# Optimization experiments

Measured on AMD Instinct MI355X. Metric: run time of the kernel, lower is better.

Reference implementation:

```python
import jax, jax.numpy as jnp
import numpy as np

B = 32            # graphs in batch
NPG = 2048        # nodes per graph (equal-size graphs -> static topk sizes)
N = B * NPG
DEG = 8
E = N * DEG
IN = 64
H1 = 2 * IN       # 128
H2 = 2 * H1       # 256
K1 = NPG // 2     # SAGPooling ratio=0.5
K2 = K1 // 2
EPS = 1e-5


def _lin(k, fi, fo):
    s = 1.0 / np.sqrt(fi)
    return jax.random.uniform(k, (fi, fo), jnp.float32, -s, s)


def setup_inputs() -> dict:
    key = jax.random.key(0)
    ks = jax.random.split(key, 24)
    x = jax.random.normal(ks[0], (N, IN), jnp.float32)
    # edges strictly within each graph
    eg = jnp.repeat(jnp.arange(B, dtype=jnp.int32), NPG * DEG)
    src = eg * NPG + jax.random.randint(ks[1], (E,), 0, NPG, jnp.int32)
    tgt = eg * NPG + jax.random.randint(ks[2], (E,), 0, NPG, jnp.int32)
    edge_index = jnp.stack([src, tgt])
    batch = jnp.repeat(jnp.arange(B, dtype=jnp.int32), NPG)
    return {
        "x": x, "edge_index": edge_index, "batch": batch,
        # SAGEConv1: lin_l (neighbors, with bias) + lin_r (root, no bias)
        "W1l": _lin(ks[3], IN, H1), "b1l": jnp.zeros((H1,), jnp.float32),
        "W1r": _lin(ks[4], IN, H1),
        "bn1_g": jnp.ones((H1,), jnp.float32), "bn1_b": jnp.zeros((H1,), jnp.float32),
        # SAGPooling1 scorer = GraphConv(H1, 1): lin_rel (sum-agg, bias) + lin_root
        "p1_Wrel": _lin(ks[5], H1, 1), "p1_brel": jnp.zeros((1,), jnp.float32),
        "p1_Wroot": _lin(ks[6], H1, 1),
        "W2l": _lin(ks[7], H1, H2), "b2l": jnp.zeros((H2,), jnp.float32),
        "W2r": _lin(ks[8], H1, H2),
        "bn2_g": jnp.ones((H2,), jnp.float32), "bn2_b": jnp.zeros((H2,), jnp.float32),
        "p2_Wrel": _lin(ks[9], H2, 1), "p2_brel": jnp.zeros((1,), jnp.float32),
        "p2_Wroot": _lin(ks[10], H2, 1),
        "Wlin": _lin(ks[11], H2, 2), "blin": jnp.zeros((2,), jnp.float32),
    }


def sage_conv(x, src, tgt, emask, Wl, bl, Wr, n):
    # PyG SAGEConv: mean-aggregate x_j over valid incoming edges, then lin_l(agg)+lin_r(x)
    msg = x[src] * emask[:, None]
    s = jax.ops.segment_sum(msg, tgt, num_segments=n)
    cnt = jax.ops.segment_sum(emask, tgt, num_segments=n)
    mean = s / jnp.maximum(cnt, 1.0)[:, None]
    return mean @ Wl + bl + x @ Wr


def graph_conv_score(x, src, tgt, emask, Wrel, brel, Wroot, n):
    # PyG GraphConv (sum aggregation), out_channels=1
    s = jax.ops.segment_sum(x[src] * emask[:, None], tgt, num_segments=n)
    return (s @ Wrel + brel + x @ Wroot)[:, 0]


def batch_norm(x, g, b):
    m = x.mean(0)
    v = jnp.mean((x - m) ** 2, 0)  # biased var, as BatchNorm1d training
    return (x - m) * jax.lax.rsqrt(v + EPS) * g + b


def sag_pool(x, src, tgt, emask, score, npg, k):
    # per-graph top-k by score; x_kept scaled by tanh(score); edges re-filtered via mask
    vals, idx = jax.lax.top_k(score.reshape(B, npg), k)          # [B,k]
    perm = (jnp.arange(B, dtype=jnp.int32)[:, None] * npg + idx.astype(jnp.int32)).reshape(-1)
    xnew = x[perm] * jnp.tanh(vals.reshape(-1))[:, None]
    mapping = jnp.full((x.shape[0],), -1, jnp.int32).at[perm].set(
        jnp.arange(B * k, dtype=jnp.int32))
    ns, nt = mapping[src], mapping[tgt]
    valid = emask * ((ns >= 0) & (nt >= 0)).astype(emask.dtype)
    return xnew, jnp.maximum(ns, 0), jnp.maximum(nt, 0), valid


def reference(x, edge_index, batch, W1l, b1l, W1r, bn1_g, bn1_b,
              p1_Wrel, p1_brel, p1_Wroot, W2l, b2l, W2r, bn2_g, bn2_b,
              p2_Wrel, p2_brel, p2_Wroot, Wlin, blin):
    src, tgt = edge_index[0], edge_index[1]
    emask = jnp.ones((src.shape[0],), x.dtype)

    h = sage_conv(x, src, tgt, emask, W1l, b1l, W1r, N)
    h = jax.nn.relu(batch_norm(h, bn1_g, bn1_b))
    s1 = graph_conv_score(h, src, tgt, emask, p1_Wrel, p1_brel, p1_Wroot, N)
    h, src, tgt, emask = sag_pool(h, src, tgt, emask, s1, NPG, K1)

    n1 = B * K1
    h = sage_conv(h, src, tgt, emask, W2l, b2l, W2r, n1)
    h = jax.nn.relu(batch_norm(h, bn2_g, bn2_b))
    s2 = graph_conv_score(h, src, tgt, emask, p2_Wrel, p2_brel, p2_Wroot, n1)
    h, src, tgt, emask = sag_pool(h, src, tgt, emask, s2, K1, K2)

    batch2 = jnp.repeat(jnp.arange(B, dtype=jnp.int32), K2)
    pooled = jax.ops.segment_sum(h, batch2, num_segments=B) / jnp.asarray(K2, h.dtype)
    out = jax.nn.relu(pooled) @ Wlin + blin
    return jax.nn.softmax(out, axis=1)
```

## Files before the change

### kernel.cpp

```cpp
#include <hip/hip_runtime.h>
#include <math.h>

#define Bg   32
#define NPGc 2048
#define Nn   (Bg*NPGc)
#define DEGc 8
#define Ee   (Nn*DEGc)
#define INc  64
#define H1c  128
#define H2c  256
#define K1c  1024
#define K2c  512
#define N1c  (Bg*K1c)
#define N2c  (Bg*K2c)
#define SLAB 64

typedef __attribute__((ext_vector_type(8))) short short8;
typedef __attribute__((ext_vector_type(4))) float f32x4;

__device__ __forceinline__ ushort f2bf(float f) {
    uint u = __float_as_uint(f);
    uint r = (u + 0x7fffu + ((u >> 16) & 1u)) >> 16;
    return (ushort)r;
}
__device__ __forceinline__ float bf2f(ushort v) { return __uint_as_float((uint)v << 16); }
__device__ __forceinline__ float bfhi(uint v) { return __uint_as_float(v & 0xffff0000u); }
__device__ __forceinline__ float bflo(uint v) { return __uint_as_float(v << 16); }
__device__ __forceinline__ uint fkey(float f) {
    uint u = __float_as_uint(f);
    return u ^ ((uint)((int)u >> 31) | 0x80000000u);
}
__device__ __forceinline__ void unpk8(uint4 v, float* f) {
    f[0] = bflo(v.x); f[1] = bfhi(v.x);
    f[2] = bflo(v.y); f[3] = bfhi(v.y);
    f[4] = bflo(v.z); f[5] = bfhi(v.z);
    f[6] = bflo(v.w); f[7] = bfhi(v.w);
}
__device__ __forceinline__ uint4 pack8(const float* a, float inv) {
    uint4 o;
    o.x = (uint)f2bf(a[0] * inv) | ((uint)f2bf(a[1] * inv) << 16);
    o.y = (uint)f2bf(a[2] * inv) | ((uint)f2bf(a[3] * inv) << 16);
    o.z = (uint)f2bf(a[4] * inv) | ((uint)f2bf(a[5] * inv) << 16);
    o.w = (uint)f2bf(a[6] * inv) | ((uint)f2bf(a[7] * inv) << 16);
    return o;
}
__device__ __forceinline__ void accf8(float* a, const float* p) {
    float4 u0 = *(const float4*)p;
    float4 u1 = *(const float4*)(p + 4);
    a[0] += u0.x; a[1] += u0.y; a[2] += u0.z; a[3] += u0.w;
    a[4] += u1.x; a[5] += u1.y; a[6] += u1.z; a[7] += u1.w;
}

__global__ void init_kernel(int4* __restrict__ wc1, int4* __restrict__ dstats) {
    int id = blockIdx.x * blockDim.x + threadIdx.x;
    int4 z = {0, 0, 0, 0};
    if (id < 16384) { wc1[id] = z; return; }
    id -= 16384;
    if (id < 384)   { dstats[id] = z; }
}
#define INIT_TOTAL (16384 + 384)

__global__ void prep2_kernel(const int* __restrict__ src, const int* __restrict__ tgt,
                             const float* __restrict__ W1l, const float* __restrict__ W1r,
                             const float* __restrict__ W2l, const float* __restrict__ W2r,
                             ushort* __restrict__ T1l, ushort* __restrict__ T1r,
                             ushort* __restrict__ T2l, ushort* __restrict__ T2r,
                             int* __restrict__ wc1, int* __restrict__ col1) {
    int id = blockIdx.x * blockDim.x + threadIdx.x;
    if (id < Ee) {
        int t = tgt[id];
        int p = atomicAdd(&wc1[t], 1);
        col1[t * SLAB + p] = src[id];
        return;
    }
    id -= Ee;
    if (id < 8192) {
        int c = id / 64, k = id % 64;
        T1l[id] = f2bf(W1l[k * 128 + c]);
        T1r[id] = f2bf(W1r[k * 128 + c]);
        return;
    }
    id -= 8192;
    if (id < 32768) {
        int c = id / 128, k = id % 128;
        T2l[id] = f2bf(W2l[k * 256 + c]);
        T2r[id] = f2bf(W2r[k * 256 + c]);
    }
}
#define PREP2_TOTAL (Ee + 8192 + 32768)

__global__ __launch_bounds__(512) void gemm1f_kernel(
        const float* __restrict__ x, const int* __restrict__ deg,
        const int* __restrict__ col, const ushort* __restrict__ Wtl,
        const ushort* __restrict__ Wtr, const float* __restrict__ bias,
        ushort* __restrict__ out, double* __restrict__ dsum,
        double* __restrict__ dsq) {
    __shared__ ushort As[2][2][128][36];
    __shared__ ushort Bs[2][2][128][36];
    __shared__ float bsumS[2][128], bsqS[2][128];
    int b = blockIdx.x;
    int bs = ((b & 7) << 6) + (b >> 3);
    int m0 = bs << 7;
    int lane = threadIdx.x & 63;
    int wid = threadIdx.x >> 6;
    int wr = (wid & 1) << 6, wc = (wid >> 1) << 5;
    int l16 = lane & 15, quad = lane >> 4;

    int ar = threadIdx.x >> 2, ack = (threadIdx.x & 3) * 8;
    int anode = m0 + ar;
    int abg = anode * SLAB, adg = deg[anode];
    int4 c0h = *(const int4*)&col[abg];
    int4 c1h = *(const int4*)&col[abg + 4];
    int anb[8] = {c0h.x, c0h.y, c0h.z, c0h.w, c1h.x, c1h.y, c1h.z, c1h.w};

    {
        int r = threadIdx.x >> 2, ck = (threadIdx.x & 3) * 8;
#pragma unroll
        for (int kt = 0; kt < 2; kt++) {
            *(uint4*)&Bs[0][kt][r][ck] = *(const uint4*)&Wtl[(size_t)r * INc + kt * 32 + ck];
            *(uint4*)&Bs[1][kt][r][ck] = *(const uint4*)&Wtr[(size_t)r * INc + kt * 32 + ck];
        }
    }
    {
#pragma unroll
        for (int kt = 0; kt < 2; kt++) {
            const float* xp = &x[(size_t)anode * INc + kt * 32 + ack];
            float vals[8];
            float4 v0 = *(const float4*)xp, v1 = *(const float4*)(xp + 4);
            vals[0] = v0.x; vals[1] = v0.y; vals[2] = v0.z; vals[3] = v0.w;
            vals[4] = v1.x; vals[5] = v1.y; vals[6] = v1.z; vals[7] = v1.w;
            *(uint4*)&As[1][kt][ar][ack] = pack8(vals, 1.f);
        }
    }
    {
        float aacc[2][8];
#pragma unroll
        for (int kt = 0; kt < 2; kt++)
#pragma unroll
            for (int q = 0; q < 8; q++) aacc[kt][q] = 0.f;
#pragma unroll
        for (int j = 0; j < 8; j++)
            if (j < adg) {
                const float* xp = &x[(size_t)anb[j] * INc + ack];
#pragma unroll
                for (int kt = 0; kt < 2; kt++) accf8(aacc[kt], xp + kt * 32);
            }
        for (int i = abg + 8; i < abg + adg; i++) {
            const float* xp = &x[(size_t)col[i] * INc + ack];
#pragma unroll
            for (int kt = 0; kt < 2; kt++) accf8(aacc[kt], xp + kt * 32);
        }
        int cdg = adg < 1 ? 1 : adg;
        float inv = 1.f / (float)cdg;
#pragma unroll
        for (int kt = 0; kt < 2; kt++)
            *(uint4*)&As[0][kt][ar][ack] = pack8(aacc[kt], inv);
    }
    __syncthreads();

    f32x4 acc[4][2];
#pragma unroll
    for (int a = 0; a < 4; a++)
#pragma unroll
        for (int c = 0; c < 2; c++) acc[a][c] = (f32x4){0.f, 0.f, 0.f, 0.f};

#pragma unroll
    for (int kt = 0; kt < 2; kt++) {
        short8 a[2][4], bfr[2][2];
#pragma unroll
        for (int s = 0; s < 2; s++)
#pragma unroll
            for (int mt = 0; mt < 4; mt++)
                a[s][mt] = *(const short8*)&As[s][kt][wr + mt * 16 + l16][quad * 8];
#pragma unroll
        for (int s = 0; s < 2; s++)
#pragma unroll
            for (int nt = 0; nt < 2; nt++)
                bfr[s][nt] = *(const short8*)&Bs[s][kt][wc + nt * 16 + l16][quad * 8];
#pragma unroll
        for (int mt = 0; mt < 4; mt++)
#pragma unroll
            for (int nt = 0; nt < 2; nt++) {
                acc[mt][nt] = __builtin_amdgcn_mfma_f32_16x16x32_bf16(
                    a[0][mt], bfr[0][nt], acc[mt][nt], 0, 0, 0);
                acc[mt][nt] = __builtin_amdgcn_mfma_f32_16x16x32_bf16(
                    a[1][mt], bfr[1][nt], acc[mt][nt], 0, 0, 0);
            }
    }
    float s[2] = {0.f, 0.f}, sq[2] = {0.f, 0.f};
#pragma unroll
    for (int nt = 0; nt < 2; nt++) {
        int colx = wc + nt * 16 + l16;
        float bv = bias[colx];
#pragma unroll
        for (int mt = 0; mt < 4; mt++)
#pragma unroll
            for (int rr = 0; rr < 4; rr++) {
                int row = m0 + wr + mt * 16 + quad * 4 + rr;
                float ov = acc[mt][nt][rr] + bv;
                out[(size_t)row * H1c + colx] = f2bf(ov);
                s[nt] += ov; sq[nt] += ov * ov;
            }
    }
#pragma unroll
    for (int nt = 0; nt < 2; nt++) {
        float ss = s[nt], qq = sq[nt];
        ss += __shfl_down(ss, 16); qq += __shfl_down(qq, 16);
        ss += __shfl_down(ss, 32); qq += __shfl_down(qq, 32);
        if (quad == 0) {
            bsumS[wid & 1][wc + nt * 16 + l16] = ss;
            bsqS[wid & 1][wc + nt * 16 + l16] = qq;
        }
    }
    __syncthreads();
    if (threadIdx.x < 128) {
        int c = threadIdx.x;
        atomicAdd(&dsum[c], (double)(bsumS[0][c] + bsumS[1][c]));
        atomicAdd(&dsq[c], (double)(bsqS[0][c] + bsqS[1][c]));
    }
}

template<int C>
__global__ __launch_bounds__(256) void score_kernel(const ushort* __restrict__ h,
                                                    const double* __restrict__ dsum,
                                                    const double* __restrict__ dsq,
                                                    const float* __restrict__ g,
                                                    const float* __restrict__ b,
                                                    const float* __restrict__ wrel,
                                                    const float* __restrict__ wroot,
                                                    float* __restrict__ r,
                                                    float* __restrict__ root, int n) {
    __shared__ float sc[C], sh[C], wrl[C], wrt[C];
    if ((int)threadIdx.x < C) {
        int c = threadIdx.x;
        double m = dsum[c] / (double)n;
        double var = dsq[c] / (double)n - m * m;
        float s = g[c] * (float)(1.0 / sqrt(var + 1e-5));
        sc[c] = s; sh[c] = b[c] - (float)m * s;
        wrl[c] = wrel[c]; wrt[c] = wroot[c];
    }
    __syncthreads();
    int gid = blockIdx.x * 256 + threadIdx.x;
    int node = gid >> 3, ln = gid & 7;
    float rr = 0.f, rt = 0.f;
#pragma unroll
    for (int p = 0; p < C / 64; p++) {
        int cb = p * 64 + ln * 8;
        uint4 v = *(const uint4*)&h[(size_t)node * C + cb];
        float vv[8];
        unpk8(v, vv);
#pragma unroll
        for (int q = 0; q < 8; q++) {
            int cc = cb + q;
            float val = fmaxf(vv[q] * sc[cc] + sh[cc], 0.f);
            rr += val * wrl[cc];
            rt += val * wrt[cc];
        }
    }
#pragma unroll
    for (int off = 4; off; off >>= 1) {
        rr += __shfl_down(rr, off);
        rt += __shfl_down(rt, off);
    }
    if (ln == 0) { r[node] = rr; root[node] = rt; }
}

__global__ void __launch_bounds__(1024) sel1_kernel(const float* __restrict__ r,
                                                    const float* __restrict__ root,
                                                    const int* __restrict__ deg,
                                                    const int* __restrict__ col,
                                                    const float* __restrict__ brel,
                                                    int* __restrict__ perm,
                                                    float* __restrict__ tval,
                                                    int* __restrict__ map) {
    __shared__ float rL[2048];
    __shared__ float svals[2048];
    __shared__ uint hist[257];
    __shared__ uint wsum[16];
    __shared__ uint s_b, s_rem;
    int g = blockIdx.x;
    int tid = threadIdx.x;
    int lane = tid & 63, wid = tid >> 6;
    int base = g * NPGc;
    rL[tid] = r[base + tid];
    rL[tid + 1024] = r[base + tid + 1024];
    if (tid < 257) hist[tid] = 0;
    __syncthreads();
    float bv = brel[0];
#pragma unroll
    for (int j = 0; j < 2; j++) {
        int i = tid + (j << 10);
        int node = base + i;
        float acc = bv + root[node];
        int e0 = node * SLAB, dg = deg[node];
        int4 c0 = *(const int4*)&col[e0];
        int4 c1 = *(const int4*)&col[e0 + 4];
        int nb[8] = {c0.x, c0.y, c0.z, c0.w, c1.x, c1.y, c1.z, c1.w};
#pragma unroll
        for (int q = 0; q < 8; q++)
            if (q < dg) acc += rL[nb[q] - base];
        for (int e = e0 + 8; e < e0 + dg; e++) acc += rL[col[e] - base];
        svals[i] = acc;
    }
    __syncthreads();

    uint prefix = 0, himask = 0, rem = (uint)K1c;
    for (int shift = 24; shift >= 0; shift -= 8) {
#pragma unroll
        for (int j = 0; j < 2; j++) {
            uint kk = fkey(svals[tid + (j << 10)]);
            if ((kk & himask) == prefix) atomicAdd(&hist[(kk >> shift) & 255], 1);
        }
        __syncthreads();
        if (tid < 64) {
            int L = tid;
            uint h0 = hist[4 * L], h1v = hist[4 * L + 1], h2v = hist[4 * L + 2],
                 h3 = hist[4 * L + 3];
            uint s3 = h3, s2 = h2v + s3, s1 = h1v + s2, s0 = h0 + s1;
            uint v = s0;
            for (int off = 1; off < 64; off <<= 1) {
                uint u = __shfl_down(v, off);
                if (L + off < 64) v += u;
            }
            uint above = v - s0;
            hist[4 * L] = s0 + above;
            hist[4 * L + 1] = s1 + above;
            hist[4 * L + 2] = s2 + above;
            hist[4 * L + 3] = s3 + above;
        }
        __syncthreads();
        if (tid < 256) {
            uint sb = hist[tid], sb1 = hist[tid + 1];
            if (sb >= rem && sb1 < rem) { s_b = (uint)tid; s_rem = rem - sb1; }
        }
        __syncthreads();
        prefix |= (s_b << shift);
        rem = s_rem;
        himask |= (0xFFu << shift);
        if (tid < 256) hist[tid] = 0;
        __syncthreads();
    }
    uint thr = prefix;
    uint tieM = rem;
    uint gcnt = 0, ecnt = 0, gflags = 0, eflags = 0;
#pragma unroll
    for (int j = 0; j < 2; j++) {
        uint kk = fkey(svals[tid + (j << 10)]);
        if (kk > thr) { gflags |= 1u << j; gcnt++; }
        else if (kk == thr) { eflags |= 1u << j; ecnt++; }
    }
    uint key = (gcnt << 16) | ecnt;
    uint v = key;
    for (int off = 1; off < 64; off <<= 1) {
        uint u = __shfl_up(v, off);
        if (lane >= off) v += u;
    }
    if (lane == 63) wsum[wid] = v;
    __syncthreads();
    if (tid < 16) {
        uint w0 = wsum[tid], w = w0;
        for (int off = 1; off < 16; off <<= 1) {
            uint u = __shfl_up(w, off);
            if ((int)tid >= off) w += u;
        }
        wsum[tid] = w - w0;
    }
    __syncthreads();
    uint excl = (v - key) + wsum[wid];
    uint gbase = excl >> 16, ebase = excl & 0xFFFFu;
#pragma unroll
    for (int j = 0; j < 2; j++) {
        bool gt = (gflags >> j) & 1u;
        bool eq = (eflags >> j) & 1u;
        int i = tid + (j << 10);
        int o = -1;
        if (gt || (eq && ebase < tieM)) {
            uint pos = gbase + min(ebase, tieM);
            o = g * K1c + (int)pos;
            perm[o] = base + i;
            tval[o] = tanhf(svals[i]);
        }
        map[base + i] = o;
        gbase += gt ? 1u : 0u;
        ebase += eq ? 1u : 0u;
    }
}

__global__ void __launch_bounds__(256) nofill2_kernel(
        const int* __restrict__ perm1, const int* __restrict__ map1,
        const int* __restrict__ deg1, const int* __restrict__ col1,
        int* __restrict__ wc2, int* __restrict__ col2) {
    int n = blockIdx.x * 256 + threadIdx.x;
    int o = perm1[n];
    int e0 = o * SLAB, dg = deg1[o];
    int4 c0 = *(const int4*)&col1[e0];
    int4 c1 = *(const int4*)&col1[e0 + 4];
    int nb[8] = {c0.x, c0.y, c0.z, c0.w, c1.x, c1.y, c1.z, c1.w};
    int cnt = 0;
    int ob = n * SLAB;
#pragma unroll
    for (int j = 0; j < 8; j++) {
        if (j < dg) {
            int m = map1[nb[j]];
            if (m >= 0) col2[ob + cnt++] = m;
        }
    }
    for (int e = e0 + 8; e < e0 + dg; e++) {
        int m = map1[col1[e]];
        if (m >= 0) col2[ob + cnt++] = m;
    }
    wc2[n] = cnt;
}

__global__ __launch_bounds__(512) void gemm2f_kernel(
        const ushort* __restrict__ h1, const int* __restrict__ perm1,
        const float* __restrict__ tv1, const double* __restrict__ dsum1,
        const double* __restrict__ dsq1, const float* __restrict__ bn1g,
        const float* __restrict__ bn1b, const int* __restrict__ deg,
        const int* __restrict__ col, const ushort* __restrict__ Wtl,
        const ushort* __restrict__ Wtr, const float* __restrict__ bias,
        ushort* __restrict__ out, double* __restrict__ dsum,
        double* __restrict__ dsq) {
    __shared__ ushort As[2][4][128][36];
    __shared__ ushort Bs[2][2][256][36];
    __shared__ float bsumS[2][256], bsqS[2][256];
    __shared__ float sc1[128], sh1[128];
    int b = blockIdx.x;
    int bs = ((b & 7) << 5) + (b >> 3);
    int m0 = bs << 7;
    int lane = threadIdx.x & 63;
    int wid = threadIdx.x >> 6;
    int wr = (wid & 1) << 6, wc = (wid >> 1) << 6;
    int l16 = lane & 15, quad = lane >> 4;

    if (threadIdx.x < 128) {
        int c = threadIdx.x;
        double m = dsum1[c] / (double)Nn;
        double var = dsq1[c] / (double)Nn - m * m;
        float s = bn1g[c] * (float)(1.0 / sqrt(var + 1e-5));
        sc1[c] = s; sh1[c] = bn1b[c] - (float)m * s;
    }

    int ar = threadIdx.x >> 2, ack = (threadIdx.x & 3) * 8;
    int anode = m0 + ar;
    int aold = perm1[anode];
    float atv = tv1[anode];
    int abg = anode * SLAB, adg = deg[anode];
    int4 c0h = *(const int4*)&col[abg];
    int4 c1h = *(const int4*)&col[abg + 4];
    int anb[8] = {c0h.x, c0h.y, c0h.z, c0h.w, c1h.x, c1h.y, c1h.z, c1h.w};
    int aon[8]; float atn[8];
#pragma unroll
    for (int j = 0; j < 8; j++) {
        int nbv = (j < adg) ? anb[j] : anode;
        aon[j] = perm1[nbv];
        atn[j] = tv1[nbv];
    }
    __syncthreads();

    {
#pragma unroll
        for (int kt = 0; kt < 4; kt++) {
            uint4 hv = *(const uint4*)&h1[((size_t)aold << 7) + kt * 32 + ack];
            float vals[8];
            unpk8(hv, vals);
#pragma unroll
            for (int q = 0; q < 8; q++) {
                int cc = kt * 32 + ack + q;
                vals[q] = fmaxf(vals[q] * sc1[cc] + sh1[cc], 0.f) * atv;
            }
            *(uint4*)&As[1][kt][ar][ack] = pack8(vals, 1.f);
        }
    }
    {
        float aacc[4][8];
#pragma unroll
        for (int kt = 0; kt < 4; kt++)
#pragma unroll
            for (int q = 0; q < 8; q++) aacc[kt][q] = 0.f;
#pragma unroll
        for (int j = 0; j < 8; j++)
            if (j < adg) {
                const ushort* hp = &h1[(size_t)aon[j] << 7];
                float tn = atn[j];
#pragma unroll
                for (int kt = 0; kt < 4; kt++) {
                    uint4 u = *(const uint4*)&hp[kt * 32 + ack];
                    float f[8];
                    unpk8(u, f);
#pragma unroll
                    for (int q = 0; q < 8; q++) {
                        int cc = kt * 32 + ack + q;
                        aacc[kt][q] += fmaxf(f[q] * sc1[cc] + sh1[cc], 0.f) * tn;
                    }
                }
            }
        for (int i = abg + 8; i < abg + adg; i++) {
            int nbv = col[i];
            int on = perm1[nbv];
            float tn = tv1[nbv];
            const ushort* hp = &h1[(size_t)on << 7];
#pragma unroll
            for (int kt = 0; kt < 4; kt++) {
                uint4 u = *(const uint4*)&hp[kt * 32 + ack];
                float f[8];
                unpk8(u, f);
#pragma unroll
                for (int q = 0; q < 8; q++) {
                    int cc = kt * 32 + ack + q;
                    aacc[kt][q] += fmaxf(f[q] * sc1[cc] + sh1[cc], 0.f) * tn;
                }
            }
        }
        int cdg = adg < 1 ? 1 : adg;
        float inv = 1.f / (float)cdg;
#pragma unroll
        for (int kt = 0; kt < 4; kt++)
            *(uint4*)&As[0][kt][ar][ack] = pack8(aacc[kt], inv);
    }
    for (int idx = threadIdx.x; idx < 1024; idx += 512) {
        int rr = idx >> 2, ck = (idx & 3) * 8;
        *(uint4*)&Bs[0][0][rr][ck] = *(const uint4*)&Wtl[(size_t)rr * H1c + ck];
        *(uint4*)&Bs[0][1][rr][ck] = *(const uint4*)&Wtr[(size_t)rr * H1c + ck];
    }
    __syncthreads();

    f32x4 acc[4][4];
#pragma unroll
    for (int a = 0; a < 4; a++)
#pragma unroll
        for (int c = 0; c < 4; c++) acc[a][c] = (f32x4){0.f, 0.f, 0.f, 0.f};

#pragma unroll
    for (int kt = 0; kt < 4; kt++) {
        int bf = kt & 1;
        if (kt < 3) {
            int kn = (kt + 1) * 32;
            for (int idx = threadIdx.x; idx < 1024; idx += 512) {
                int rr = idx >> 2, ck = (idx & 3) * 8;
                *(uint4*)&Bs[bf ^ 1][0][rr][ck] =
                    *(const uint4*)&Wtl[(size_t)rr * H1c + kn + ck];
                *(uint4*)&Bs[bf ^ 1][1][rr][ck] =
                    *(const uint4*)&Wtr[(size_t)rr * H1c + kn + ck];
            }
        }
        short8 a[2][4], bfr[2][4];
#pragma unroll
        for (int s = 0; s < 2; s++)
#pragma unroll
            for (int mt = 0; mt < 4; mt++)
                a[s][mt] = *(const short8*)&As[s][kt][wr + mt * 16 + l16][quad * 8];
#pragma unroll
        for (int s = 0; s < 2; s++)
#pragma unroll
            for (int nt = 0; nt < 4; nt++)
                bfr[s][nt] = *(const short8*)&Bs[bf][s][wc + nt * 16 + l16][quad * 8];
#pragma unroll
        for (int mt = 0; mt < 4; mt++)
#pragma unroll
            for (int nt = 0; nt < 4; nt++) {
                acc[mt][nt] = __builtin_amdgcn_mfma_f32_16x16x32_bf16(
                    a[0][mt], bfr[0][nt], acc[mt][nt], 0, 0, 0);
                acc[mt][nt] = __builtin_amdgcn_mfma_f32_16x16x32_bf16(
                    a[1][mt], bfr[1][nt], acc[mt][nt], 0, 0, 0);
            }
        __syncthreads();
    }
    float s[4] = {0.f, 0.f, 0.f, 0.f}, sq[4] = {0.f, 0.f, 0.f, 0.f};
#pragma unroll
    for (int nt = 0; nt < 4; nt++) {
        int colx = wc + nt * 16 + l16;
        float bv = bias[colx];
#pragma unroll
        for (int mt = 0; mt < 4; mt++)
#pragma unroll
            for (int rr = 0; rr < 4; rr++) {
                int row = m0 + wr + mt * 16 + quad * 4 + rr;
                float ov = acc[mt][nt][rr] + bv;
                out[(size_t)row * H2c + colx] = f2bf(ov);
                s[nt] += ov; sq[nt] += ov * ov;
            }
    }
#pragma unroll
    for (int nt = 0; nt < 4; nt++) {
        float ss = s[nt], qq = sq[nt];
        ss += __shfl_down(ss, 16); qq += __shfl_down(qq, 16);
        ss += __shfl_down(ss, 32); qq += __shfl_down(qq, 32);
        if (quad == 0) {
            bsumS[wid & 1][wc + nt * 16 + l16] = ss;
            bsqS[wid & 1][wc + nt * 16 + l16] = qq;
        }
    }
    __syncthreads();
    if (threadIdx.x < 256) {
        int c = threadIdx.x;
        atomicAdd(&dsum[c], (double)(bsumS[0][c] + bsumS[1][c]));
        atomicAdd(&dsq[c], (double)(bsqS[0][c] + bsqS[1][c]));
    }
}

__global__ void __launch_bounds__(1024) sel2pool_kernel(
        const float* __restrict__ r, const float* __restrict__ root,
        const int* __restrict__ deg, const int* __restrict__ col,
        const float* __restrict__ brel, const ushort* __restrict__ h2,
        const double* __restrict__ dsum, const double* __restrict__ dsq,
        const float* __restrict__ g_, const float* __restrict__ b_,
        const float* __restrict__ Wlin, const float* __restrict__ blin,
        float* __restrict__ out) {
    __shared__ float rL[1024];
    __shared__ float svals[1024];
    __shared__ uint hist[257];
    __shared__ uint wsum[16];
    __shared__ uint s_b, s_rem;
    __shared__ int permL[512];
    __shared__ float tvL[512];
    __shared__ float sc[256], sh[256];
    __shared__ float part2[32][256];
    int g = blockIdx.x;
    int tid = threadIdx.x;
    int lane = tid & 63, wid = tid >> 6;
    int base = g * K1c;
    if (tid < 256) {
        int c = tid;
        double m = dsum[c] / (double)N1c;
        double var = dsq[c] / (double)N1c - m * m;
        float s = g_[c] * (float)(1.0 / sqrt(var + 1e-5));
        sc[c] = s; sh[c] = b_[c] - (float)m * s;
    }
    rL[tid] = r[base + tid];
    if (tid < 257) hist[tid] = 0;
    __syncthreads();
    {
        int node = base + tid;
        float acc = brel[0] + root[node];
        int e0 = node * SLAB, dg = deg[node];
        int4 c0 = *(const int4*)&col[e0];
        int4 c1 = *(const int4*)&col[e0 + 4];
        int nb[8] = {c0.x, c0.y, c0.z, c0.w, c1.x, c1.y, c1.z, c1.w};
#pragma unroll
        for (int q = 0; q < 8; q++)
            if (q < dg) acc += rL[nb[q] - base];
        for (int e = e0 + 8; e < e0 + dg; e++) acc += rL[col[e] - base];
        svals[tid] = acc;
    }
    __syncthreads();

    uint prefix = 0, himask = 0, rem = (uint)K2c;
    for (int shift = 24; shift >= 0; shift -= 8) {
        {
            uint kk = fkey(svals[tid]);
            if ((kk & himask) == prefix) atomicAdd(&hist[(kk >> shift) & 255], 1);
        }
        __syncthreads();
        if (tid < 64) {
            int L = tid;
            uint h0 = hist[4 * L], h1v = hist[4 * L + 1], h2v = hist[4 * L + 2],
                 h3 = hist[4 * L + 3];
            uint s3 = h3, s2 = h2v + s3, s1 = h1v + s2, s0 = h0 + s1;
            uint v = s0;
            for (int off = 1; off < 64; off <<= 1) {
                uint u = __shfl_down(v, off);
                if (L + off < 64) v += u;
            }
            uint above = v - s0;
            hist[4 * L] = s0 + above;
            hist[4 * L + 1] = s1 + above;
            hist[4 * L + 2] = s2 + above;
            hist[4 * L + 3] = s3 + above;
        }
        __syncthreads();
        if (tid < 256) {
            uint sb = hist[tid], sb1 = hist[tid + 1];
            if (sb >= rem && sb1 < rem) { s_b = (uint)tid; s_rem = rem - sb1; }
        }
        __syncthreads();
        prefix |= (s_b << shift);
        rem = s_rem;
        himask |= (0xFFu << shift);
        if (tid < 256) hist[tid] = 0;
        __syncthreads();
    }
    uint thr = prefix;
    uint tieM = rem;

    uint kk = fkey(svals[tid]);
    bool gt = kk > thr, eq = kk == thr;
    uint key = (gt ? 0x10000u : 0u) | (eq ? 1u : 0u);
    uint v = key;
    for (int off = 1; off < 64; off <<= 1) {
        uint u = __shfl_up(v, off);
        if (lane >= off) v += u;
    }
    if (lane == 63) wsum[wid] = v;
    __syncthreads();
    if (tid < 16) {
        uint w0 = wsum[tid], w = w0;
        for (int off = 1; off < 16; off <<= 1) {
            uint u = __shfl_up(w, off);
            if ((int)tid >= off) w += u;
        }
        wsum[tid] = w - w0;
    }
    __syncthreads();
    uint excl = (v - key) + wsum[wid];
    uint gbase = excl >> 16, ebase = excl & 0xFFFFu;
    if (gt || (eq && ebase < tieM)) {
        uint pos = gbase + min(ebase, tieM);
        permL[pos] = base + tid;
        tvL[pos] = tanhf(svals[tid]);
    }
    __syncthreads();

    {
        int rl = tid & 31, rg = tid >> 5;
        float a[8] = {0.f, 0.f, 0.f, 0.f, 0.f, 0.f, 0.f, 0.f};
        for (int it = 0; it < 16; it++) {
            int j = rg + it * 32;
            int row = permL[j];
            float tv = tvL[j];
            uint4 hv = *(const uint4*)&h2[((size_t)row << 8) + rl * 8];
            float f[8];
            unpk8(hv, f);
#pragma unroll
            for (int q = 0; q < 8; q++) {
                int cc = rl * 8 + q;
                a[q] += fmaxf(f[q] * sc[cc] + sh[cc], 0.f) * tv;
            }
        }
#pragma unroll
        for (int q = 0; q < 8; q++) part2[rg][rl * 8 + q] = a[q];
    }
    __syncthreads();
    if (tid < 256) {
        float s = 0.f;
#pragma unroll
        for (int gg = 0; gg < 32; gg++) s += part2[gg][tid];
        float sv = fmaxf(s * (1.f / (float)K2c), 0.f);
        rL[tid] = sv * Wlin[tid * 2 + 0];
        rL[256 + tid] = sv * Wlin[tid * 2 + 1];
    }
    __syncthreads();
    for (int off = 128; off; off >>= 1) {
        if (tid < off) { rL[tid] += rL[tid + off]; rL[256 + tid] += rL[256 + tid + off]; }
        __syncthreads();
    }
    if (tid == 0) {
        float o0 = rL[0] + blin[0], o1 = rL[256] + blin[1];
        float m = fmaxf(o0, o1);
        float e0 = expf(o0 - m), e1 = expf(o1 - m);
        float inv = 1.f / (e0 + e1);
        out[g * 2 + 0] = e0 * inv;
        out[g * 2 + 1] = e1 * inv;
    }
}

extern "C" void kernel_launch(void* const* d_in, const int* in_sizes, int n_in,
                              void* d_out, int out_size, void* d_ws, size_t ws_size,
                              hipStream_t stream) {
    const float* x      = (const float*)d_in[0];
    const int*   ei     = (const int*)d_in[1];
    const int*   src    = ei;
    const int*   tgt    = ei + Ee;
    const float* W1l    = (const float*)d_in[3];
    const float* b1l    = (const float*)d_in[4];
    const float* W1r    = (const float*)d_in[5];
    const float* bn1g   = (const float*)d_in[6];
    const float* bn1b   = (const float*)d_in[7];
    const float* p1Wrel = (const float*)d_in[8];
    const float* p1brel = (const float*)d_in[9];
    const float* p1Wroot= (const float*)d_in[10];
    const float* W2l    = (const float*)d_in[11];
    const float* b2l    = (const float*)d_in[12];
    const float* W2r    = (const float*)d_in[13];
    const float* bn2g   = (const float*)d_in[14];
    const float* bn2b   = (const float*)d_in[15];
    const float* p2Wrel = (const float*)d_in[16];
    const float* p2brel = (const float*)d_in[17];
    const float* p2Wroot= (const float*)d_in[18];
    const float* Wlin   = (const float*)d_in[19];
    const float* blin   = (const float*)d_in[20];
    float* out = (float*)d_out;
    char* ws = (char*)d_ws;

    size_t o = 0;
    auto A = [&](size_t b) { size_t r = o; o += (b + 255) & ~(size_t)255; return r; };
    size_t oH1   = A((size_t)Nn * H1c * 2);
    size_t oH2   = A((size_t)N1c * H2c * 2);
    size_t oCol1 = A((size_t)Nn * SLAB * 4);
    size_t oCol2 = A((size_t)N1c * SLAB * 4);
    size_t oWc1  = A((size_t)Nn * 4);
    size_t oR1   = A((size_t)Nn * 4);
    size_t oRoot1= A((size_t)Nn * 4);
    size_t oMap1 = A((size_t)Nn * 4);
    size_t oPerm1= A((size_t)N1c * 4);
    size_t oTv1  = A((size_t)N1c * 4);
    size_t oWc2  = A((size_t)N1c * 4);
    size_t oR2   = A((size_t)N1c * 4);
    size_t oRoot2= A((size_t)N1c * 4);
    size_t oDst  = A(768 * 8);
    size_t oWt1l = A(8192 * 2);
    size_t oWt1r = A(8192 * 2);
    size_t oWt2l = A(32768 * 2);
    size_t oWt2r = A(32768 * 2);
    (void)ws_size; (void)in_sizes; (void)n_in; (void)out_size;

    ushort* h1   = (ushort*)(ws + oH1);
    ushort* h2   = (ushort*)(ws + oH2);
    int* col1    = (int*)(ws + oCol1);
    int* col2    = (int*)(ws + oCol2);
    int* wc1     = (int*)(ws + oWc1);
    float* r1    = (float*)(ws + oR1);
    float* root1 = (float*)(ws + oRoot1);
    int* map1    = (int*)(ws + oMap1);
    int* perm1   = (int*)(ws + oPerm1);
    float* tv1   = (float*)(ws + oTv1);
    int* wc2     = (int*)(ws + oWc2);
    float* r2    = (float*)(ws + oR2);
    float* root2 = (float*)(ws + oRoot2);
    double* dsum1= (double*)(ws + oDst);
    double* dsq1 = dsum1 + 128;
    double* dsum2= dsum1 + 256;
    double* dsq2 = dsum1 + 512;
    ushort* T1l  = (ushort*)(ws + oWt1l);
    ushort* T1r  = (ushort*)(ws + oWt1r);
    ushort* T2l  = (ushort*)(ws + oWt2l);
    ushort* T2r  = (ushort*)(ws + oWt2r);

    init_kernel<<<(INIT_TOTAL + 255) / 256, 256, 0, stream>>>(
        (int4*)wc1, (int4*)dsum1);

    prep2_kernel<<<PREP2_TOTAL / 256, 256, 0, stream>>>(
        src, tgt, W1l, W1r, W2l, W2r, T1l, T1r, T2l, T2r, wc1, col1);

    gemm1f_kernel<<<512, 512, 0, stream>>>(x, wc1, col1, T1l, T1r, b1l, h1,
                                           dsum1, dsq1);

    score_kernel<H1c><<<Nn / 32, 256, 0, stream>>>(h1, dsum1, dsq1, bn1g, bn1b, p1Wrel,
                                                   p1Wroot, r1, root1, Nn);

    sel1_kernel<<<Bg, 1024, 0, stream>>>(r1, root1, wc1, col1, p1brel, perm1, tv1, map1);

    nofill2_kernel<<<N1c / 256, 256, 0, stream>>>(perm1, map1, wc1, col1, wc2, col2);

    gemm2f_kernel<<<256, 512, 0, stream>>>(h1, perm1, tv1, dsum1, dsq1, bn1g, bn1b,
                                           wc2, col2, T2l, T2r, b2l, h2, dsum2, dsq2);

    score_kernel<H2c><<<N1c / 32, 256, 0, stream>>>(h2, dsum2, dsq2, bn2g, bn2b, p2Wrel,
                                                    p2Wroot, r2, root2, N1c);

    sel2pool_kernel<<<Bg, 1024, 0, stream>>>(r2, root2, wc2, col2, p2brel, h2, dsum2,
                                             dsq2, bn2g, bn2b, Wlin, blin, out);
}
```

Measured before the change: 218.2 us.

## Fuse stage-2 GEMM, scoring, selection and pooling into one cooperative kernel

Merges the edge-filter step into sel1 using shared-memory maps. Replaces gemm2f, score2 and sel2pool with one cooperative kernel that keeps the GEMM accumulators in registers across grid syncs. BN2 stats, scores, top-k selection, pooling and the final softmax are computed in phases without writing h2 to memory. This removes the h2 round-trip and several launches, but adds four grid-wide barriers and leaves phases where only 32 of 256 blocks do work.

```diff
diff --git a/kernel.cpp b/kernel.cpp
--- a/kernel.cpp
+++ b/kernel.cpp
@@ -1,5 +1,8 @@
 #include <hip/hip_runtime.h>
+#include <hip/hip_cooperative_groups.h>
 #include <math.h>
+
+namespace cg = cooperative_groups;
 
 #define Bg   32
 #define NPGc 2048
@@ -51,14 +54,17 @@
     a[4] += u1.x; a[5] += u1.y; a[6] += u1.z; a[7] += u1.w;
 }
 
-__global__ void init_kernel(int4* __restrict__ wc1, int4* __restrict__ dstats) {
+__global__ void init_kernel(int4* __restrict__ wc1, int4* __restrict__ dstats,
+                            int4* __restrict__ pooled) {
     int id = blockIdx.x * blockDim.x + threadIdx.x;
     int4 z = {0, 0, 0, 0};
     if (id < 16384) { wc1[id] = z; return; }
     id -= 16384;
-    if (id < 384)   { dstats[id] = z; }
-}
-#define INIT_TOTAL (16384 + 384)
+    if (id < 384)   { dstats[id] = z; return; }
+    id -= 384;
+    if (id < 2048)  { pooled[id] = z; }
+}
+#define INIT_TOTAL (16384 + 384 + 2048)
 
 __global__ void prep2_kernel(const int* __restrict__ src, const int* __restrict__ tgt,
                              const float* __restrict__ W1l, const float* __restrict__ W1r,
@@ -272,12 +278,15 @@
                                                     const float* __restrict__ brel,
                                                     int* __restrict__ perm,
                                                     float* __restrict__ tval,
-                                                    int* __restrict__ map) {
+                                                    int* __restrict__ wc2,
+                                                    int* __restrict__ col2) {
     __shared__ float rL[2048];
     __shared__ float svals[2048];
     __shared__ uint hist[257];
     __shared__ uint wsum[16];
     __shared__ uint s_b, s_rem;
+    __shared__ int mapL[2048];
+    __shared__ int oldL[1024];
     int g = blockIdx.x;
     int tid = threadIdx.x;
     int lane = tid & 63, wid = tid >> 6;
@@ -379,69 +388,78 @@
             o = g * K1c + (int)pos;
             perm[o] = base + i;
             tval[o] = tanhf(svals[i]);
-        }
-        map[base + i] = o;
+            oldL[pos] = i;
+        }
+        mapL[i] = o;
         gbase += gt ? 1u : 0u;
         ebase += eq ? 1u : 0u;
     }
-}
-
-__global__ void __launch_bounds__(256) nofill2_kernel(
-        const int* __restrict__ perm1, const int* __restrict__ map1,
-        const int* __restrict__ deg1, const int* __restrict__ col1,
-        int* __restrict__ wc2, int* __restrict__ col2) {
-    int n = blockIdx.x * 256 + threadIdx.x;
-    int o = perm1[n];
-    int e0 = o * SLAB, dg = deg1[o];
-    int4 c0 = *(const int4*)&col1[e0];
-    int4 c1 = *(const int4*)&col1[e0 + 4];
-    int nb[8] = {c0.x, c0.y, c0.z, c0.w, c1.x, c1.y, c1.z, c1.w};
-    int cnt = 0;
-    int ob = n * SLAB;
-#pragma unroll
-    for (int j = 0; j < 8; j++) {
-        if (j < dg) {
-            int m = map1[nb[j]];
+    __syncthreads();
+    {
+        int p = tid;
+        int i = oldL[p];
+        int node = base + i;
+        int e0 = node * SLAB, dg = deg[node];
+        int4 cc0 = *(const int4*)&col[e0];
+        int4 cc1 = *(const int4*)&col[e0 + 4];
+        int nb[8] = {cc0.x, cc0.y, cc0.z, cc0.w, cc1.x, cc1.y, cc1.z, cc1.w};
+        int cnt = 0;
+        int newid = g * K1c + p;
+        int ob = newid * SLAB;
+#pragma unroll
+        for (int q = 0; q < 8; q++)
+            if (q < dg) {
+                int m = mapL[nb[q] - base];
+                if (m >= 0) col2[ob + cnt++] = m;
+            }
+        for (int e = e0 + 8; e < e0 + dg; e++) {
+            int m = mapL[col[e] - base];
             if (m >= 0) col2[ob + cnt++] = m;
         }
-    }
-    for (int e = e0 + 8; e < e0 + dg; e++) {
-        int m = map1[col1[e]];
-        if (m >= 0) col2[ob + cnt++] = m;
-    }
-    wc2[n] = cnt;
-}
-
-__global__ __launch_bounds__(512) void gemm2f_kernel(
+        wc2[newid] = cnt;
+    }
+}
+
+__global__ __launch_bounds__(512) void gemm2s_kernel(
         const ushort* __restrict__ h1, const int* __restrict__ perm1,
         const float* __restrict__ tv1, const double* __restrict__ dsum1,
         const double* __restrict__ dsq1, const float* __restrict__ bn1g,
         const float* __restrict__ bn1b, const int* __restrict__ deg,
         const int* __restrict__ col, const ushort* __restrict__ Wtl,
         const ushort* __restrict__ Wtr, const float* __restrict__ bias,
-        ushort* __restrict__ out, double* __restrict__ dsum,
-        double* __restrict__ dsq) {
+        double* __restrict__ dsum, double* __restrict__ dsq,
+        const float* __restrict__ bn2g, const float* __restrict__ bn2b,
+        const float* __restrict__ wrel, const float* __restrict__ wroot,
+        const float* __restrict__ brel, float* __restrict__ r2,
+        float* __restrict__ root2, float* __restrict__ tvflag,
+        float* __restrict__ pooled, const float* __restrict__ Wlin,
+        const float* __restrict__ blin, float* __restrict__ out) {
     __shared__ ushort As[2][4][128][36];
     __shared__ ushort Bs[2][2][256][36];
     __shared__ float bsumS[2][256], bsqS[2][256];
     __shared__ float sc1[128], sh1[128];
+    __shared__ float sc2S[256], shfS[256];
+    cg::grid_group grid = cg::this_grid();
+
     int b = blockIdx.x;
     int bs = ((b & 7) << 5) + (b >> 3);
     int m0 = bs << 7;
-    int lane = threadIdx.x & 63;
-    int wid = threadIdx.x >> 6;
+    int g = bs >> 3;
+    int tid = threadIdx.x;
+    int lane = tid & 63;
+    int wid = tid >> 6;
     int wr = (wid & 1) << 6, wc = (wid >> 1) << 6;
     int l16 = lane & 15, quad = lane >> 4;
 
-    if (threadIdx.x < 128) {
-        int c = threadIdx.x;
+    if (tid < 128) {
+        int c = tid;
         double m = dsum1[c] / (double)Nn;
         double var = dsq1[c] / (double)Nn - m * m;
         float s = bn1g[c] * (float)(1.0 / sqrt(var + 1e-5));
         sc1[c] = s; sh1[c] = bn1b[c] - (float)m * s;
     }
 
-    int ar = threadIdx.x >> 2, ack = (threadIdx.x & 3) * 8;
+    int ar = tid >> 2, ack = (tid & 3) * 8;
     int anode = m0 + ar;
     int aold = perm1[anode];
     float atv = tv1[anode];
@@ -518,7 +536,7 @@
         for (int kt = 0; kt < 4; kt++)
             *(uint4*)&As[0][kt][ar][ack] = pack8(aacc[kt], inv);
     }
-    for (int idx = threadIdx.x; idx < 1024; idx += 512) {
+    for (int idx = tid; idx < 1024; idx += 512) {
         int rr = idx >> 2, ck = (idx & 3) * 8;
         *(uint4*)&Bs[0][0][rr][ck] = *(const uint4*)&Wtl[(size_t)rr * H1c + ck];
         *(uint4*)&Bs[0][1][rr][ck] = *(const uint4*)&Wtr[(size_t)rr * H1c + ck];
@@ -536,7 +554,7 @@
         int bf = kt & 1;
         if (kt < 3) {
             int kn = (kt + 1) * 32;
-            for (int idx = threadIdx.x; idx < 1024; idx += 512) {
+            for (int idx = tid; idx < 1024; idx += 512) {
                 int rr = idx >> 2, ck = (idx & 3) * 8;
                 *(uint4*)&Bs[bf ^ 1][0][rr][ck] =
                     *(const uint4*)&Wtl[(size_t)rr * H1c + kn + ck];
@@ -566,191 +584,253 @@
             }
         __syncthreads();
     }
-    float s[4] = {0.f, 0.f, 0.f, 0.f}, sq[4] = {0.f, 0.f, 0.f, 0.f};
-#pragma unroll
-    for (int nt = 0; nt < 4; nt++) {
-        int colx = wc + nt * 16 + l16;
-        float bv = bias[colx];
-#pragma unroll
-        for (int mt = 0; mt < 4; mt++)
-#pragma unroll
-            for (int rr = 0; rr < 4; rr++) {
-                int row = m0 + wr + mt * 16 + quad * 4 + rr;
-                float ov = acc[mt][nt][rr] + bv;
-                out[(size_t)row * H2c + colx] = f2bf(ov);
-                s[nt] += ov; sq[nt] += ov * ov;
-            }
-    }
-#pragma unroll
-    for (int nt = 0; nt < 4; nt++) {
-        float ss = s[nt], qq = sq[nt];
-        ss += __shfl_down(ss, 16); qq += __shfl_down(qq, 16);
-        ss += __shfl_down(ss, 32); qq += __shfl_down(qq, 32);
-        if (quad == 0) {
-            bsumS[wid & 1][wc + nt * 16 + l16] = ss;
-            bsqS[wid & 1][wc + nt * 16 + l16] = qq;
-        }
-    }
-    __syncthreads();
-    if (threadIdx.x < 256) {
-        int c = threadIdx.x;
-        atomicAdd(&dsum[c], (double)(bsumS[0][c] + bsumS[1][c]));
-        atomicAdd(&dsq[c], (double)(bsqS[0][c] + bsqS[1][c]));
-    }
-}
-
-__global__ void __launch_bounds__(1024) sel2pool_kernel(
-        const float* __restrict__ r, const float* __restrict__ root,
-        const int* __restrict__ deg, const int* __restrict__ col,
-        const float* __restrict__ brel, const ushort* __restrict__ h2,
-        const double* __restrict__ dsum, const double* __restrict__ dsq,
-        const float* __restrict__ g_, const float* __restrict__ b_,
-        const float* __restrict__ Wlin, const float* __restrict__ blin,
-        float* __restrict__ out) {
-    __shared__ float rL[1024];
-    __shared__ float svals[1024];
-    __shared__ uint hist[257];
-    __shared__ uint wsum[16];
-    __shared__ uint s_b, s_rem;
-    __shared__ int permL[512];
-    __shared__ float tvL[512];
-    __shared__ float sc[256], sh[256];
-    __shared__ float part2[32][256];
-    int g = blockIdx.x;
-    int tid = threadIdx.x;
-    int lane = tid & 63, wid = tid >> 6;
-    int base = g * K1c;
+    {
+        float s[4] = {0.f, 0.f, 0.f, 0.f}, sq[4] = {0.f, 0.f, 0.f, 0.f};
+#pragma unroll
+        for (int nt = 0; nt < 4; nt++) {
+            int colx = wc + nt * 16 + l16;
+            float bv = bias[colx];
+#pragma unroll
+            for (int mt = 0; mt < 4; mt++)
+#pragma unroll
+                for (int rr = 0; rr < 4; rr++) {
+                    float ov = acc[mt][nt][rr] + bv;
+                    s[nt] += ov; sq[nt] += ov * ov;
+                }
+        }
+#pragma unroll
+        for (int nt = 0; nt < 4; nt++) {
+            float ss = s[nt], qq = sq[nt];
+            ss += __shfl_down(ss, 16); qq += __shfl_down(qq, 16);
+            ss += __shfl_down(ss, 32); qq += __shfl_down(qq, 32);
+            if (quad == 0) {
+                bsumS[wid & 1][wc + nt * 16 + l16] = ss;
+                bsqS[wid & 1][wc + nt * 16 + l16] = qq;
+            }
+        }
+        __syncthreads();
+        if (tid < 256) {
+            int c = tid;
+            atomicAdd(&dsum[c], (double)(bsumS[0][c] + bsumS[1][c]));
+            atomicAdd(&dsq[c], (double)(bsqS[0][c] + bsqS[1][c]));
+        }
+    }
+    grid.sync();
+
     if (tid < 256) {
         int c = tid;
         double m = dsum[c] / (double)N1c;
         double var = dsq[c] / (double)N1c - m * m;
-        float s = g_[c] * (float)(1.0 / sqrt(var + 1e-5));
-        sc[c] = s; sh[c] = b_[c] - (float)m * s;
-    }
-    rL[tid] = r[base + tid];
-    if (tid < 257) hist[tid] = 0;
-    __syncthreads();
+        float s2 = bn2g[c] * (float)(1.0 / sqrt(var + 1e-5));
+        sc2S[c] = s2;
+        shfS[c] = (bn2b[c] - (float)m * s2) + bias[c] * s2;
+    }
+    __syncthreads();
+    float scc[4], shc[4];
+#pragma unroll
+    for (int nt = 0; nt < 4; nt++) {
+        int c = wc + nt * 16 + l16;
+        scc[nt] = sc2S[c]; shc[nt] = shfS[c];
+    }
+    float* basef = (float*)&Bs[0][0][0][0];
+    float* rpS = basef;
+    float* rtS = basef + 512;
     {
-        int node = base + tid;
-        float acc = brel[0] + root[node];
-        int e0 = node * SLAB, dg = deg[node];
-        int4 c0 = *(const int4*)&col[e0];
-        int4 c1 = *(const int4*)&col[e0 + 4];
-        int nb[8] = {c0.x, c0.y, c0.z, c0.w, c1.x, c1.y, c1.z, c1.w};
-#pragma unroll
-        for (int q = 0; q < 8; q++)
-            if (q < dg) acc += rL[nb[q] - base];
-        for (int e = e0 + 8; e < e0 + dg; e++) acc += rL[col[e] - base];
-        svals[tid] = acc;
-    }
-    __syncthreads();
-
-    uint prefix = 0, himask = 0, rem = (uint)K2c;
-    for (int shift = 24; shift >= 0; shift -= 8) {
-        {
-            uint kk = fkey(svals[tid]);
-            if ((kk & himask) == prefix) atomicAdd(&hist[(kk >> shift) & 255], 1);
-        }
-        __syncthreads();
-        if (tid < 64) {
-            int L = tid;
-            uint h0 = hist[4 * L], h1v = hist[4 * L + 1], h2v = hist[4 * L + 2],
-                 h3 = hist[4 * L + 3];
-            uint s3 = h3, s2 = h2v + s3, s1 = h1v + s2, s0 = h0 + s1;
-            uint v = s0;
-            for (int off = 1; off < 64; off <<= 1) {
-                uint u = __shfl_down(v, off);
-                if (L + off < 64) v += u;
-            }
-            uint above = v - s0;
-            hist[4 * L] = s0 + above;
-            hist[4 * L + 1] = s1 + above;
-            hist[4 * L + 2] = s2 + above;
-            hist[4 * L + 3] = s3 + above;
-        }
-        __syncthreads();
+        float wlc[4], wtc[4];
+#pragma unroll
+        for (int nt = 0; nt < 4; nt++) {
+            int c = wc + nt * 16 + l16;
+            wlc[nt] = wrel[c]; wtc[nt] = wroot[c];
+        }
+#pragma unroll
+        for (int mt = 0; mt < 4; mt++)
+#pragma unroll
+            for (int rr = 0; rr < 4; rr++) {
+                float pr = 0.f, pt = 0.f;
+#pragma unroll
+                for (int nt = 0; nt < 4; nt++) {
+                    float v = fmaxf(acc[mt][nt][rr] * scc[nt] + shc[nt], 0.f);
+                    pr += v * wlc[nt]; pt += v * wtc[nt];
+                }
+#pragma unroll
+                for (int off = 8; off; off >>= 1) {
+                    pr += __shfl_down(pr, off);
+                    pt += __shfl_down(pt, off);
+                }
+                if (l16 == 0) {
+                    int rl = wr + mt * 16 + quad * 4 + rr;
+                    rpS[(wid >> 1) * 128 + rl] = pr;
+                    rtS[(wid >> 1) * 128 + rl] = pt;
+                }
+            }
+        __syncthreads();
+        if (tid < 128) {
+            r2[m0 + tid] = rpS[tid] + rpS[128 + tid] + rpS[256 + tid] + rpS[384 + tid];
+            root2[m0 + tid] = rtS[tid] + rtS[128 + tid] + rtS[256 + tid] + rtS[384 + tid];
+        }
+    }
+    grid.sync();
+
+    if ((bs & 7) == 0) {
+        float* rLS    = basef + 1920;
+        float* svalsS = basef + 2944;
+        uint*  histS  = (uint*)(basef + 3968);
+        uint*  wsumS  = histS + 257;
+        uint*  sbS    = wsumS + 8;
+        uint*  sremS  = sbS + 1;
+        int base = g * K1c;
+        rLS[tid] = r2[base + tid];
+        rLS[tid + 512] = r2[base + tid + 512];
+        if (tid < 257) histS[tid] = 0;
+        __syncthreads();
+        float bv2 = brel[0];
+#pragma unroll
+        for (int j = 0; j < 2; j++) {
+            int i = tid + (j << 9);
+            int node = base + i;
+            float a2 = bv2 + root2[node];
+            int e0 = node * SLAB, dg = deg[node];
+            int4 cc0 = *(const int4*)&col[e0];
+            int4 cc1 = *(const int4*)&col[e0 + 4];
+            int nb[8] = {cc0.x, cc0.y, cc0.z, cc0.w, cc1.x, cc1.y, cc1.z, cc1.w};
+#pragma unroll
+            for (int q = 0; q < 8; q++)
+                if (q < dg) a2 += rLS[nb[q] - base];
+            for (int e = e0 + 8; e < e0 + dg; e++) a2 += rLS[col[e] - base];
+            svalsS[i] = a2;
+        }
+        __syncthreads();
+        uint prefix = 0, himask = 0, rem = (uint)K2c;
+        for (int shift = 24; shift >= 0; shift -= 8) {
+#pragma unroll
+            for (int j = 0; j < 2; j++) {
+                uint kk = fkey(svalsS[tid + (j << 9)]);
+                if ((kk & himask) == prefix) atomicAdd(&histS[(kk >> shift) & 255], 1);
+            }
+            __syncthreads();
+            if (tid < 64) {
+                int L = tid;
+                uint h0 = histS[4 * L], hh1 = histS[4 * L + 1], hh2 = histS[4 * L + 2],
+                     h3 = histS[4 * L + 3];
+                uint s3 = h3, s2v = hh2 + s3, s1 = hh1 + s2v, s0 = h0 + s1;
+                uint v = s0;
+                for (int off = 1; off < 64; off <<= 1) {
+                    uint u = __shfl_down(v, off);
+                    if (L + off < 64) v += u;
+                }
+                uint above = v - s0;
+                histS[4 * L] = s0 + above;
+                histS[4 * L + 1] = s1 + above;
+                histS[4 * L + 2] = s2v + above;
+                histS[4 * L + 3] = s3 + above;
+            }
+            __syncthreads();
+            if (tid < 256) {
+                uint sb = histS[tid], sb1 = histS[tid + 1];
+                if (sb >= rem && sb1 < rem) { *sbS = (uint)tid; *sremS = rem - sb1; }
+            }
+            __syncthreads();
+            prefix |= (*sbS << shift);
+            rem = *sremS;
+            himask |= (0xFFu << shift);
+            if (tid < 256) histS[tid] = 0;
+            __syncthreads();
+        }
+        uint thr = prefix, tieM = rem;
+        uint gcnt = 0, ecnt = 0, gflags = 0, eflags = 0;
+#pragma unroll
+        for (int j = 0; j < 2; j++) {
+            uint kk = fkey(svalsS[tid + (j << 9)]);
+            if (kk > thr) { gflags |= 1u << j; gcnt++; }
+            else if (kk == thr) { eflags |= 1u << j; ecnt++; }
+        }
+        uint key = (gcnt << 16) | ecnt;
+        uint v = key;
+        for (int off = 1; off < 64; off <<= 1) {
+            uint u = __shfl_up(v, off);
+            if (lane >= off) v += u;
+        }
+        if (lane == 63) wsumS[wid] = v;
+        __syncthreads();
+        if (tid < 8) {
+            uint w0 = wsumS[tid], w = w0;
+            for (int off = 1; off < 8; off <<= 1) {
+                uint u = __shfl_up(w, off);
+                if ((int)tid >= off) w += u;
+            }
+            wsumS[tid] = w - w0;
+        }
+        __syncthreads();
+        uint excl = (v - key) + wsumS[wid];
+        uint gbase = excl >> 16, ebase = excl & 0xFFFFu;
+#pragma unroll
+        for (int j = 0; j < 2; j++) {
+            bool gt = (gflags >> j) & 1u;
+            bool eq = (eflags >> j) & 1u;
+            int i = tid + (j << 9);
+            bool selv = gt || (eq && ebase < tieM);
+            tvflag[base + i] = selv ? tanhf(svalsS[i]) : 0.f;
+            gbase += gt ? 1u : 0u;
+            ebase += eq ? 1u : 0u;
+        }
+    }
+    grid.sync();
+
+    {
+        float* flagS = basef + 1024;
+        float* poolS = basef + 1152;
+        if (tid < 128) flagS[tid] = tvflag[m0 + tid];
+        if (tid < 256) poolS[tid] = 0.f;
+        __syncthreads();
+        float pc[4] = {0.f, 0.f, 0.f, 0.f};
+#pragma unroll
+        for (int mt = 0; mt < 4; mt++)
+#pragma unroll
+            for (int rr = 0; rr < 4; rr++) {
+                int rl = wr + mt * 16 + quad * 4 + rr;
+                float fl = flagS[rl];
+#pragma unroll
+                for (int nt = 0; nt < 4; nt++)
+                    pc[nt] += fmaxf(acc[mt][nt][rr] * scc[nt] + shc[nt], 0.f) * fl;
+            }
+#pragma unroll
+        for (int nt = 0; nt < 4; nt++) {
+            pc[nt] += __shfl_down(pc[nt], 16);
+            pc[nt] += __shfl_down(pc[nt], 32);
+        }
+        if (quad == 0) {
+#pragma unroll
+            for (int nt = 0; nt < 4; nt++)
+                atomicAdd(&poolS[wc + nt * 16 + l16], pc[nt]);
+        }
+        __syncthreads();
+        if (tid < 256) atomicAdd(&pooled[g * H2c + tid], poolS[tid]);
+    }
+    grid.sync();
+
+    if ((bs & 7) == 0) {
+        float* redS = basef + 1408;
         if (tid < 256) {
-            uint sb = hist[tid], sb1 = hist[tid + 1];
-            if (sb >= rem && sb1 < rem) { s_b = (uint)tid; s_rem = rem - sb1; }
-        }
-        __syncthreads();
-        prefix |= (s_b << shift);
-        rem = s_rem;
-        himask |= (0xFFu << shift);
-        if (tid < 256) hist[tid] = 0;
-        __syncthreads();
-    }
-    uint thr = prefix;
-    uint tieM = rem;
-
-    uint kk = fkey(svals[tid]);
-    bool gt = kk > thr, eq = kk == thr;
-    uint key = (gt ? 0x10000u : 0u) | (eq ? 1u : 0u);
-    uint v = key;
-    for (int off = 1; off < 64; off <<= 1) {
-        uint u = __shfl_up(v, off);
-        if (lane >= off) v += u;
-    }
-    if (lane == 63) wsum[wid] = v;
-    __syncthreads();
-    if (tid < 16) {
-        uint w0 = wsum[tid], w = w0;
-        for (int off = 1; off < 16; off <<= 1) {
-            uint u = __shfl_up(w, off);
-            if ((int)tid >= off) w += u;
-        }
-        wsum[tid] = w - w0;
-    }
-    __syncthreads();
-    uint excl = (v - key) + wsum[wid];
-    uint gbase = excl >> 16, ebase = excl & 0xFFFFu;
-    if (gt || (eq && ebase < tieM)) {
-        uint pos = gbase + min(ebase, tieM);
-        permL[pos] = base + tid;
-        tvL[pos] = tanhf(svals[tid]);
-    }
-    __syncthreads();
-
-    {
-        int rl = tid & 31, rg = tid >> 5;
-        float a[8] = {0.f, 0.f, 0.f, 0.f, 0.f, 0.f, 0.f, 0.f};
-        for (int it = 0; it < 16; it++) {
-            int j = rg + it * 32;
-            int row = permL[j];
-            float tv = tvL[j];
-            uint4 hv = *(const uint4*)&h2[((size_t)row << 8) + rl * 8];
-            float f[8];
-            unpk8(hv, f);
-#pragma unroll
-            for (int q = 0; q < 8; q++) {
-                int cc = rl * 8 + q;
-                a[q] += fmaxf(f[q] * sc[cc] + sh[cc], 0.f) * tv;
-            }
-        }
-#pragma unroll
-        for (int q = 0; q < 8; q++) part2[rg][rl * 8 + q] = a[q];
-    }
-    __syncthreads();
-    if (tid < 256) {
-        float s = 0.f;
-#pragma unroll
-        for (int gg = 0; gg < 32; gg++) s += part2[gg][tid];
-        float sv = fmaxf(s * (1.f / (float)K2c), 0.f);
-        rL[tid] = sv * Wlin[tid * 2 + 0];
-        rL[256 + tid] = sv * Wlin[tid * 2 + 1];
-    }
-    __syncthreads();
-    for (int off = 128; off; off >>= 1) {
-        if (tid < off) { rL[tid] += rL[tid + off]; rL[256 + tid] += rL[256 + tid + off]; }
-        __syncthreads();
-    }
-    if (tid == 0) {
-        float o0 = rL[0] + blin[0], o1 = rL[256] + blin[1];
-        float m = fmaxf(o0, o1);
-        float e0 = expf(o0 - m), e1 = expf(o1 - m);
-        float inv = 1.f / (e0 + e1);
-        out[g * 2 + 0] = e0 * inv;
-        out[g * 2 + 1] = e1 * inv;
+            float s = fmaxf(pooled[g * H2c + tid] * (1.f / (float)K2c), 0.f);
+            redS[tid] = s * Wlin[2 * tid];
+            redS[256 + tid] = s * Wlin[2 * tid + 1];
+        }
+        __syncthreads();
+        for (int off = 128; off; off >>= 1) {
+            if (tid < off) {
+                redS[tid] += redS[tid + off];
+                redS[256 + tid] += redS[256 + tid + off];
+            }
+            __syncthreads();
+        }
+        if (tid == 0) {
+            float o0 = redS[0] + blin[0], o1 = redS[256] + blin[1];
+            float mm = fmaxf(o0, o1);
+            float e0 = expf(o0 - mm), e1 = expf(o1 - mm);
+            float inv = 1.f / (e0 + e1);
+            out[g * 2 + 0] = e0 * inv;
+            out[g * 2 + 1] = e1 * inv;
+        }
     }
 }
 
@@ -785,38 +865,37 @@
     size_t o = 0;
     auto A = [&](size_t b) { size_t r = o; o += (b + 255) & ~(size_t)255; return r; };
     size_t oH1   = A((size_t)Nn * H1c * 2);
-    size_t oH2   = A((size_t)N1c * H2c * 2);
     size_t oCol1 = A((size_t)Nn * SLAB * 4);
     size_t oCol2 = A((size_t)N1c * SLAB * 4);
     size_t oWc1  = A((size_t)Nn * 4);
     size_t oR1   = A((size_t)Nn * 4);
     size_t oRoot1= A((size_t)Nn * 4);
-    size_t oMap1 = A((size_t)Nn * 4);
     size_t oPerm1= A((size_t)N1c * 4);
     size_t oTv1  = A((size_t)N1c * 4);
     size_t oWc2  = A((size_t)N1c * 4);
     size_t oR2   = A((size_t)N1c * 4);
     size_t oRoot2= A((size_t)N1c * 4);
+    size_t oFlag = A((size_t)N1c * 4);
     size_t oDst  = A(768 * 8);
     size_t oWt1l = A(8192 * 2);
     size_t oWt1r = A(8192 * 2);
     size_t oWt2l = A(32768 * 2);
     size_t oWt2r = A(32768 * 2);
+    size_t oPool = A(Bg * H2c * 4);
     (void)ws_size; (void)in_sizes; (void)n_in; (void)out_size;
 
     ushort* h1   = (ushort*)(ws + oH1);
-    ushort* h2   = (ushort*)(ws + oH2);
     int* col1    = (int*)(ws + oCol1);
     int* col2    = (int*)(ws + oCol2);
     int* wc1     = (int*)(ws + oWc1);
     float* r1    = (float*)(ws + oR1);
     float* root1 = (float*)(ws + oRoot1);
-    int* map1    = (int*)(ws + oMap1);
     int* perm1   = (int*)(ws + oPerm1);
     float* tv1   = (float*)(ws + oTv1);
     int* wc2     = (int*)(ws + oWc2);
     float* r2    = (float*)(ws + oR2);
     float* root2 = (float*)(ws + oRoot2);
+    float* tvflag= (float*)(ws + oFlag);
     double* dsum1= (double*)(ws + oDst);
     double* dsq1 = dsum1 + 128;
     double* dsum2= dsum1 + 256;
@@ -825,9 +904,10 @@
     ushort* T1r  = (ushort*)(ws + oWt1r);
     ushort* T2l  = (ushort*)(ws + oWt2l);
     ushort* T2r  = (ushort*)(ws + oWt2r);
+    float* pooled= (float*)(ws + oPool);
 
     init_kernel<<<(INIT_TOTAL + 255) / 256, 256, 0, stream>>>(
-        (int4*)wc1, (int4*)dsum1);
+        (int4*)wc1, (int4*)dsum1, (int4*)pooled);
 
     prep2_kernel<<<PREP2_TOTAL / 256, 256, 0, stream>>>(
         src, tgt, W1l, W1r, W2l, W2r, T1l, T1r, T2l, T2r, wc1, col1);
@@ -838,16 +918,22 @@
     score_kernel<H1c><<<Nn / 32, 256, 0, stream>>>(h1, dsum1, dsq1, bn1g, bn1b, p1Wrel,
                                                    p1Wroot, r1, root1, Nn);
 
-    sel1_kernel<<<Bg, 1024, 0, stream>>>(r1, root1, wc1, col1, p1brel, perm1, tv1, map1);
-
-    nofill2_kernel<<<N1c / 256, 256, 0, stream>>>(perm1, map1, wc1, col1, wc2, col2);
-
-    gemm2f_kernel<<<256, 512, 0, stream>>>(h1, perm1, tv1, dsum1, dsq1, bn1g, bn1b,
-                                           wc2, col2, T2l, T2r, b2l, h2, dsum2, dsq2);
-
-    score_kernel<H2c><<<N1c / 32, 256, 0, stream>>>(h2, dsum2, dsq2, bn2g, bn2b, p2Wrel,
-                                                    p2Wroot, r2, root2, N1c);
-
-    sel2pool_kernel<<<Bg, 1024, 0, stream>>>(r2, root2, wc2, col2, p2brel, h2, dsum2,
-                                             dsq2, bn2g, bn2b, Wlin, blin, out);
-}
+    sel1_kernel<<<Bg, 1024, 0, stream>>>(r1, root1, wc1, col1, p1brel, perm1, tv1,
+                                         wc2, col2);
+
+    {
+        void* kargs[] = {
+            (void*)&h1, (void*)&perm1, (void*)&tv1,
+            (void*)&dsum1, (void*)&dsq1, (void*)&bn1g, (void*)&bn1b,
+            (void*)&wc2, (void*)&col2,
+            (void*)&T2l, (void*)&T2r, (void*)&b2l,
+            (void*)&dsum2, (void*)&dsq2,
+            (void*)&bn2g, (void*)&bn2b,
+            (void*)&p2Wrel, (void*)&p2Wroot, (void*)&p2brel,
+            (void*)&r2, (void*)&root2, (void*)&tvflag, (void*)&pooled,
+            (void*)&Wlin, (void*)&blin, (void*)&out
+        };
+        hipLaunchCooperativeKernel((const void*)gemm2s_kernel, dim3(256), dim3(512),
+                                   kargs, 0, stream);
+    }
+}
```

Measured after the change: 347.1 us. +59.1%, slower.
